# Performance work log

Hardware: AMD Instinct MI355X
Metric: run time of the kernel (lower is better)

Reference implementation:

```python
import jax, jax.numpy as jnp
import numpy as np

CHUNK = 128
TAU = 0.7


def setup_inputs() -> dict:
    key = jax.random.key(0)
    ks = jax.random.split(key, 8)
    B, S, D, H, E = 4, 4096, 2048, 1024, 8
    x = jax.random.normal(ks[0], (B, S, D), dtype=jnp.float32)
    prev_expert_indices = jax.random.randint(ks[1], (B,), 0, E)
    # router MLP params (stored as [in, out]); xavier-uniform-like init, zero biases
    def xavier(k, fin, fout):
        lim = np.sqrt(6.0 / (fin + fout)).astype(np.float32)
        return jax.random.uniform(k, (fin, fout), jnp.float32, -lim, lim)
    w1 = xavier(ks[2], D, H)
    b1 = jnp.zeros((H,), jnp.float32)
    w2 = xavier(ks[3], H, H // 2)
    b2 = jnp.zeros((H // 2,), jnp.float32)
    w3 = jax.random.normal(ks[4], (H // 2, E), jnp.float32) * 0.02  # final layer std=0.02
    b3 = jnp.zeros((E,), jnp.float32)
    return {"x": x, "prev_expert_indices": prev_expert_indices,
            "w1": w1, "b1": b1, "w2": w2, "b2": b2, "w3": w3, "b3": b3}


def reference(x, prev_expert_indices, w1, b1, w2, b2, w3, b3):
    B, S, D = x.shape
    E = w3.shape[1]
    C = S // CHUNK  # num_chunks (seq_len divisible by chunk_size)

    # Router MLP on every token (Dropout is identity in eval), then per-chunk mean
    h = jax.nn.relu(x @ w1 + b1)
    h = jax.nn.relu(h @ w2 + b2)
    tok_logits = h @ w3 + b3                                   # [B, S, E]
    chunk_logits = tok_logits.reshape(B, C, CHUNK, E).mean(2)  # [B, C, E]

    top = jnp.argmax(chunk_logits, axis=-1).astype(jnp.int32)  # [B, C]

    # Sequential hysteresis over chunks (prev_expert_indices given => hysteresis active)
    def step(prev, inp):
        logits_c, top_c, is_first = inp  # [B,E], [B], scalar bool
        cur = jnp.take_along_axis(logits_c, top_c[:, None], axis=1)[:, 0]
        pv = jnp.take_along_axis(logits_c, prev[:, None], axis=1)[:, 0]
        switch = (cur - pv) > TAU
        final = jnp.where(is_first, top_c, jnp.where(switch, top_c, prev))
        flips = jnp.where(is_first, 0, switch.sum().astype(jnp.int32))
        return final, (final, flips)

    is_first = jnp.arange(C) == 0
    _, (experts_t, flips_t) = jax.lax.scan(
        step, jnp.zeros((B,), jnp.int32),
        (chunk_logits.transpose(1, 0, 2), top.T, is_first))
    expert_indices = experts_t.T                               # [B, C]

    one_hot = jax.nn.one_hot(expert_indices, E, dtype=jnp.float32)  # [B, C, E]
    routing_weights = jnp.broadcast_to(one_hot[:, :, None, :],
                                       (B, C, CHUNK, E)).reshape(B, S, E)

    # Stats
    probs = jax.nn.softmax(chunk_logits, axis=-1)
    gate_entropy = -(probs * jnp.log(probs + 1e-8)).sum(-1).mean()
    expert_utilization = one_hot.mean((0, 1))                  # [E]
    flip_rate = flips_t.sum().astype(jnp.float32) / (B * max(1, C - 1))
    routing_concentration = jnp.linalg.norm(expert_utilization)

    return (routing_weights, expert_indices, chunk_logits,
            gate_entropy, expert_utilization, flip_rate, routing_concentration)
```

## Files before the change

kernel.cpp:

```cpp
#include <hip/hip_runtime.h>
#include <math.h>

typedef _Float16 half_t;
typedef __attribute__((ext_vector_type(4))) _Float16 half4v;
typedef __attribute__((ext_vector_type(8))) _Float16 half8v;
typedef __attribute__((ext_vector_type(4))) float floatx4;

constexpr int B_ = 4, S_ = 4096, D_ = 2048, H_ = 1024, H2_ = 512, E_ = 8;
constexpr int CHUNK_ = 128;
constexpr int C_ = S_ / CHUNK_;
constexpr int M_ = B_ * S_;
constexpr float TAU_ = 0.7f;
constexpr float WSCALE = 64.0f, OSCALE = 1.0f / 64.0f;

constexpr int OUT_RW = 0;
constexpr int OUT_EI = OUT_RW + B_ * S_ * E_;
constexpr int OUT_CL = OUT_EI + B_ * C_;
constexpr int OUT_GE = OUT_CL + B_ * C_ * E_;
constexpr int OUT_UT = OUT_GE + 1;
constexpr int OUT_FR = OUT_UT + E_;
constexpr int OUT_RC = OUT_FR + 1;

__global__ __launch_bounds__(256)
void transpose_f16_kernel(const float* __restrict__ W, half_t* __restrict__ outT,
                          int K, int N)
{
    __shared__ float tile[32][33];
    const int tx = threadIdx.x & 31;
    const int ty = threadIdx.x >> 5;
    const int k0 = blockIdx.y * 32;
    const int n0 = blockIdx.x * 32;
#pragma unroll
    for (int r = 0; r < 4; ++r)
        tile[ty + r * 8][tx] = W[(size_t)(k0 + ty + r * 8) * N + n0 + tx];
    __syncthreads();
#pragma unroll
    for (int r = 0; r < 4; ++r)
        outT[(size_t)(n0 + ty + r * 8) * K + k0 + tx] = (half_t)tile[tx][ty + r * 8];
}

__global__ __launch_bounds__(256)
void transpose_split_kernel(const float* __restrict__ W, half_t* __restrict__ hi,
                            half_t* __restrict__ lo, int K, int N)
{
    __shared__ float tile[32][33];
    const int tx = threadIdx.x & 31;
    const int ty = threadIdx.x >> 5;
    const int k0 = blockIdx.y * 32;
    const int n0 = blockIdx.x * 32;
#pragma unroll
    for (int r = 0; r < 4; ++r)
        tile[ty + r * 8][tx] = W[(size_t)(k0 + ty + r * 8) * N + n0 + tx];
    __syncthreads();
#pragma unroll
    for (int r = 0; r < 4; ++r) {
        const float v = tile[tx][ty + r * 8] * WSCALE;
        const half_t h = (half_t)v;
        const size_t off = (size_t)(n0 + ty + r * 8) * K + k0 + tx;
        hi[off] = h;
        lo[off] = (half_t)(v - (float)h);
    }
}

__global__ __launch_bounds__(256, 3)
void gemm1_kernel(const float* __restrict__ X,
                  const half_t* __restrict__ BTh,
                  const float* __restrict__ bias, half_t* __restrict__ outh)
{
    constexpr int KD = D_, ND = H_, BK = 32;
    __shared__ __align__(16) half_t sA[128 * BK];
    __shared__ __align__(16) half_t sB[128 * BK];

    const int tid = threadIdx.x;
    const int lane = tid & 63;
    const int wave = tid >> 6;
    const int wm = (wave & 1) * 64;
    const int wn = (wave >> 1) * 64;
    const int rowBlk = blockIdx.x * 16 + (blockIdx.y >> 3);
    const int colBlk = blockIdx.y & 7;
    const long blockM = (long)rowBlk * 128;
    const long blockN = (long)colBlk * 128;

    floatx4 acc[4][4];
#pragma unroll
    for (int i = 0; i < 4; ++i)
#pragma unroll
        for (int j = 0; j < 4; ++j) acc[i][j] = (floatx4){0.f, 0.f, 0.f, 0.f};

    const int srow = tid >> 2;
    const int skoff = (tid & 3) * 8;
    const int ldsoff = srow * BK + skoff;
    const int fr = lane & 15;
    const int fq = (lane >> 4) * 8;

    const float* Xrow0 = X + (size_t)(blockM + srow) * KD + skoff;
    const float* Xrow1 = Xrow0 + (size_t)64 * KD;

    for (int k0 = 0; k0 < KD; k0 += BK) {
        const float4 a00 = *(const float4*)(Xrow0 + k0);
        const float4 a01 = *(const float4*)(Xrow0 + k0 + 4);
        const float4 a10 = *(const float4*)(Xrow1 + k0);
        const float4 a11 = *(const float4*)(Xrow1 + k0 + 4);
        __syncthreads();
#pragma unroll
        for (int p = 0; p < 2; ++p) {
            const size_t boff = (size_t)(blockN + srow + p * 64) * KD + k0 + skoff;
            __builtin_amdgcn_global_load_lds(
                (const __attribute__((address_space(1))) void*)(BTh + boff),
                (__attribute__((address_space(3))) void*)(sB + ldsoff + p * 2048), 16, 0, 0);
        }
        half8v h0, h1v;
        h0.s0 = (half_t)a00.x; h0.s1 = (half_t)a00.y; h0.s2 = (half_t)a00.z; h0.s3 = (half_t)a00.w;
        h0.s4 = (half_t)a01.x; h0.s5 = (half_t)a01.y; h0.s6 = (half_t)a01.z; h0.s7 = (half_t)a01.w;
        h1v.s0 = (half_t)a10.x; h1v.s1 = (half_t)a10.y; h1v.s2 = (half_t)a10.z; h1v.s3 = (half_t)a10.w;
        h1v.s4 = (half_t)a11.x; h1v.s5 = (half_t)a11.y; h1v.s6 = (half_t)a11.z; h1v.s7 = (half_t)a11.w;
        *(half8v*)(sA + ldsoff) = h0;
        *(half8v*)(sA + ldsoff + 2048) = h1v;
        __syncthreads();

        half8v fb[4];
#pragma unroll
        for (int t = 0; t < 4; ++t)
            fb[t] = *(const half8v*)(sB + (wn + t * 16 + fr) * BK + fq);
#pragma unroll
        for (int i = 0; i < 4; ++i) {
            const half8v fa = *(const half8v*)(sA + (wm + i * 16 + fr) * BK + fq);
#pragma unroll
            for (int j = 0; j < 4; ++j)
                acc[i][j] = __builtin_amdgcn_mfma_f32_16x16x32_f16(fa, fb[j], acc[i][j], 0, 0, 0);
        }
    }

    const int orow = (lane >> 4) * 4;
    const int ocol = lane & 15;
#pragma unroll
    for (int j = 0; j < 4; ++j) {
        const long gn = blockN + wn + j * 16 + ocol;
        const float bj = bias[gn];
#pragma unroll
        for (int i = 0; i < 4; ++i) {
#pragma unroll
            for (int r = 0; r < 4; ++r) {
                const float v = fmaxf(acc[i][j][r] + bj, 0.0f);
                const size_t off = (size_t)(blockM + wm + i * 16 + orow + r) * ND + gn;
                outh[off] = (half_t)v;
            }
        }
    }
}

__global__ __launch_bounds__(256, 3)
void gemm2_fused_kernel(const half_t* __restrict__ Ah,
                        const half_t* __restrict__ BTh, const half_t* __restrict__ BTl,
                        const float* __restrict__ bias, const float* __restrict__ w3,
                        float* __restrict__ cl_acc)
{
    constexpr int KD = H_, BK = 32;
    __shared__ __align__(16) half_t sAh[128 * BK];
    __shared__ __align__(16) half_t sBh[128 * BK];
    __shared__ __align__(16) half_t sBl[128 * BK];

    const int tid = threadIdx.x;
    const int lane = tid & 63;
    const int wave = tid >> 6;
    const int wm = (wave & 1) * 64;
    const int wn = (wave >> 1) * 64;
    const int d = blockIdx.y * 4 + blockIdx.x;
    const int xcd = d & 7;
    const int l = d >> 3;
    const int rowBlk = xcd * 16 + (l >> 2);
    const int colBlk = l & 3;
    const long blockM = (long)rowBlk * 128;
    const long blockN = (long)colBlk * 128;

    floatx4 acc[4][4];
#pragma unroll
    for (int i = 0; i < 4; ++i)
#pragma unroll
        for (int j = 0; j < 4; ++j) acc[i][j] = (floatx4){0.f, 0.f, 0.f, 0.f};

    const int srow = tid >> 2;
    const int skoff = (tid & 3) * 8;
    const int ldsoff = srow * BK + skoff;
    const int fr = lane & 15;
    const int fq = (lane >> 4) * 8;

    for (int k0 = 0; k0 < KD; k0 += BK) {
        __syncthreads();
#pragma unroll
        for (int p = 0; p < 2; ++p) {
            const int row = srow + p * 64;
            const size_t aoff = (size_t)(blockM + row) * KD + k0 + skoff;
            const size_t boff = (size_t)(blockN + row) * KD + k0 + skoff;
            const int loff = ldsoff + p * 2048;
            __builtin_amdgcn_global_load_lds(
                (const __attribute__((address_space(1))) void*)(Ah + aoff),
                (__attribute__((address_space(3))) void*)(sAh + loff), 16, 0, 0);
            __builtin_amdgcn_global_load_lds(
                (const __attribute__((address_space(1))) void*)(BTh + boff),
                (__attribute__((address_space(3))) void*)(sBh + loff), 16, 0, 0);
            __builtin_amdgcn_global_load_lds(
                (const __attribute__((address_space(1))) void*)(BTl + boff),
                (__attribute__((address_space(3))) void*)(sBl + loff), 16, 0, 0);
        }
        __syncthreads();

        half8v fbh[4], fbl[4];
#pragma unroll
        for (int t = 0; t < 4; ++t) {
            fbh[t] = *(const half8v*)(sBh + (wn + t * 16 + fr) * BK + fq);
            fbl[t] = *(const half8v*)(sBl + (wn + t * 16 + fr) * BK + fq);
        }
#pragma unroll
        for (int i = 0; i < 4; ++i) {
            const half8v fah = *(const half8v*)(sAh + (wm + i * 16 + fr) * BK + fq);
#pragma unroll
            for (int j = 0; j < 4; ++j) {
                acc[i][j] = __builtin_amdgcn_mfma_f32_16x16x32_f16(fah, fbh[j], acc[i][j], 0, 0, 0);
                acc[i][j] = __builtin_amdgcn_mfma_f32_16x16x32_f16(fah, fbl[j], acc[i][j], 0, 0, 0);
            }
        }
    }

    const int ocol = lane & 15;
    float p[E_];
#pragma unroll
    for (int e = 0; e < E_; ++e) p[e] = 0.0f;
#pragma unroll
    for (int j = 0; j < 4; ++j) {
        const int gn = (int)blockN + wn + j * 16 + ocol;
        const float bj = bias[gn];
        const float4 w3a = *(const float4*)(w3 + (size_t)gn * E_);
        const float4 w3b = *(const float4*)(w3 + (size_t)gn * E_ + 4);
        float colsum = 0.0f;
#pragma unroll
        for (int i = 0; i < 4; ++i)
#pragma unroll
            for (int r = 0; r < 4; ++r)
                colsum += fmaxf(acc[i][j][r] * OSCALE + bj, 0.0f);
        p[0] += colsum * w3a.x; p[1] += colsum * w3a.y;
        p[2] += colsum * w3a.z; p[3] += colsum * w3a.w;
        p[4] += colsum * w3b.x; p[5] += colsum * w3b.y;
        p[6] += colsum * w3b.z; p[7] += colsum * w3b.w;
    }
#pragma unroll
    for (int e = 0; e < E_; ++e)
#pragma unroll
        for (int off = 32; off > 0; off >>= 1)
            p[e] += __shfl_xor(p[e], off);
#pragma unroll
    for (int e = 0; e < E_; ++e)
        if (lane == e) atomicAdd(&cl_acc[rowBlk * E_ + e], p[e]);
}

__global__ __launch_bounds__(128)
void finalize_kernel(const float* __restrict__ cl_acc, const float* __restrict__ b3,
                     float* __restrict__ out, int* __restrict__ experts_ws)
{
    __shared__ float cl[B_ * C_][E_];
    __shared__ int tops[B_ * C_];
    __shared__ int finals[B_ * C_];
    __shared__ int flips[B_];
    __shared__ float ent[B_ * C_];

    const int tid = threadIdx.x;

    {
        int best = 0;
        float bvv = -1e30f;
#pragma unroll
        for (int e = 0; e < E_; ++e) {
            const float v = cl_acc[tid * E_ + e] * (1.0f / CHUNK_) + b3[e];
            cl[tid][e] = v;
            out[OUT_CL + tid * E_ + e] = v;
            if (v > bvv) { bvv = v; best = e; }
        }
        tops[tid] = best;
    }
    __syncthreads();

    if (tid < B_) {
        const int b = tid;
        int prev = 0, fl = 0;
        for (int c = 0; c < C_; ++c) {
            const int t = tops[b * C_ + c];
            int fin;
            if (c == 0) {
                fin = t;
            } else {
                const float cur = cl[b * C_ + c][t];
                const float pv = cl[b * C_ + c][prev];
                const bool sw = (cur - pv) > TAU_;
                if (sw) fl++;
                fin = sw ? t : prev;
            }
            finals[b * C_ + c] = fin;
            prev = fin;
        }
        flips[b] = fl;
    }

    {
        float m = cl[tid][0];
        for (int e = 1; e < E_; ++e) m = fmaxf(m, cl[tid][e]);
        float pr[E_], s = 0.0f;
        for (int e = 0; e < E_; ++e) { pr[e] = expf(cl[tid][e] - m); s += pr[e]; }
        const float inv = 1.0f / s;
        float h = 0.0f;
        for (int e = 0; e < E_; ++e) { const float pe = pr[e] * inv; h -= pe * logf(pe + 1e-8f); }
        ent[tid] = h;
    }
    __syncthreads();

    if (tid == 0) {
        float esum = 0.0f;
        for (int i = 0; i < B_ * C_; ++i) esum += ent[i];
        out[OUT_GE] = esum / (float)(B_ * C_);

        int cnt[E_];
        for (int e = 0; e < E_; ++e) cnt[e] = 0;
        for (int i = 0; i < B_ * C_; ++i) cnt[finals[i]]++;
        float n2 = 0.0f;
        for (int e = 0; e < E_; ++e) {
            const float u = (float)cnt[e] / (float)(B_ * C_);
            out[OUT_UT + e] = u;
            n2 += u * u;
        }
        const int totfl = flips[0] + flips[1] + flips[2] + flips[3];
        out[OUT_FR] = (float)totfl / (float)(B_ * (C_ - 1));
        out[OUT_RC] = sqrtf(n2);
    }

    out[OUT_EI + tid] = (float)finals[tid];
    experts_ws[tid] = finals[tid];
}

__global__ __launch_bounds__(256)
void routing_weights_kernel(const int* __restrict__ experts_ws, float* __restrict__ out)
{
    const int tok = blockIdx.x * 256 + threadIdx.x;
    const int b = tok >> 12;
    const int c = (tok & (S_ - 1)) >> 7;
    const int e = experts_ws[b * C_ + c];
    float4 v0 = make_float4(e == 0 ? 1.f : 0.f, e == 1 ? 1.f : 0.f,
                            e == 2 ? 1.f : 0.f, e == 3 ? 1.f : 0.f);
    float4 v1 = make_float4(e == 4 ? 1.f : 0.f, e == 5 ? 1.f : 0.f,
                            e == 6 ? 1.f : 0.f, e == 7 ? 1.f : 0.f);
    float4* dst = (float4*)(out + (size_t)tok * E_);
    dst[0] = v0;
    dst[1] = v1;
}

extern "C" void kernel_launch(void* const* d_in, const int* in_sizes, int n_in,
                              void* d_out, int out_size, void* d_ws, size_t ws_size,
                              hipStream_t stream)
{
    const float* x  = (const float*)d_in[0];
    const float* w1 = (const float*)d_in[2];
    const float* b1 = (const float*)d_in[3];
    const float* w2 = (const float*)d_in[4];
    const float* b2 = (const float*)d_in[5];
    const float* w3 = (const float*)d_in[6];
    const float* b3 = (const float*)d_in[7];
    float* out = (float*)d_out;

    half_t* w1t  = (half_t*)d_ws;
    half_t* h1h  = w1t + (size_t)H_ * D_;
    half_t* w2th = h1h + (size_t)M_ * H_;
    half_t* w2tl = w2th + (size_t)H2_ * H_;
    float*  cl_acc = (float*)(w2tl + (size_t)H2_ * H_);
    int* experts_ws = (int*)(cl_acc + B_ * C_ * E_);

    hipMemsetAsync(cl_acc, 0, (size_t)B_ * C_ * E_ * sizeof(float), stream);

    transpose_f16_kernel<<<dim3(H_ / 32, D_ / 32), dim3(256), 0, stream>>>(w1, w1t, D_, H_);
    transpose_split_kernel<<<dim3(H2_ / 32, H_ / 32), dim3(256), 0, stream>>>(w2, w2th, w2tl, H_, H2_);
    gemm1_kernel<<<dim3(H_ / 128, M_ / 128), dim3(256), 0, stream>>>(x, w1t, b1, h1h);
    gemm2_fused_kernel<<<dim3(H2_ / 128, M_ / 128), dim3(256), 0, stream>>>(
        h1h, w2th, w2tl, b2, w3, cl_acc);
    finalize_kernel<<<dim3(1), dim3(128), 0, stream>>>(cl_acc, b3, out, experts_ws);
    routing_weights_kernel<<<dim3(M_ / 256), dim3(256), 0, stream>>>(experts_ws, out + OUT_RW);
}
```

Baseline: 367.2 us.

## Merge prep/finalize kernels and prefetch next X tile in GEMM1

Fuses the two weight-transpose kernels and the accumulator memset into one prep kernel, and merges the finalize and routing-weight kernels into one kernel where every block recomputes the hysteresis scan redundantly. It also software-prefetches the next K-slice of X into registers in gemm1 so global loads overlap the MFMA work. The aim is fewer launches and less exposed load latency, at the cost of redundant per-block scan work and extra register pressure in gemm1.

Result: no change. 364.9 us (-0.6%).

```diff
diff --git a/kernel.cpp b/kernel.cpp
--- a/kernel.cpp
+++ b/kernel.cpp
@@ -2,7 +2,6 @@
 #include <math.h>
 
 typedef _Float16 half_t;
-typedef __attribute__((ext_vector_type(4))) _Float16 half4v;
 typedef __attribute__((ext_vector_type(8))) _Float16 half8v;
 typedef __attribute__((ext_vector_type(4))) float floatx4;
 
@@ -22,43 +21,43 @@
 constexpr int OUT_RC = OUT_FR + 1;
 
 __global__ __launch_bounds__(256)
-void transpose_f16_kernel(const float* __restrict__ W, half_t* __restrict__ outT,
-                          int K, int N)
+void prep_kernel(const float* __restrict__ w1, const float* __restrict__ w2,
+                 half_t* __restrict__ w1t, half_t* __restrict__ w2th,
+                 half_t* __restrict__ w2tl, float* __restrict__ cl_acc)
 {
     __shared__ float tile[32][33];
     const int tx = threadIdx.x & 31;
     const int ty = threadIdx.x >> 5;
-    const int k0 = blockIdx.y * 32;
-    const int n0 = blockIdx.x * 32;
-#pragma unroll
-    for (int r = 0; r < 4; ++r)
-        tile[ty + r * 8][tx] = W[(size_t)(k0 + ty + r * 8) * N + n0 + tx];
-    __syncthreads();
-#pragma unroll
-    for (int r = 0; r < 4; ++r)
-        outT[(size_t)(n0 + ty + r * 8) * K + k0 + tx] = (half_t)tile[tx][ty + r * 8];
-}
-
-__global__ __launch_bounds__(256)
-void transpose_split_kernel(const float* __restrict__ W, half_t* __restrict__ hi,
-                            half_t* __restrict__ lo, int K, int N)
-{
-    __shared__ float tile[32][33];
-    const int tx = threadIdx.x & 31;
-    const int ty = threadIdx.x >> 5;
-    const int k0 = blockIdx.y * 32;
-    const int n0 = blockIdx.x * 32;
-#pragma unroll
-    for (int r = 0; r < 4; ++r)
-        tile[ty + r * 8][tx] = W[(size_t)(k0 + ty + r * 8) * N + n0 + tx];
-    __syncthreads();
-#pragma unroll
-    for (int r = 0; r < 4; ++r) {
-        const float v = tile[tx][ty + r * 8] * WSCALE;
-        const half_t h = (half_t)v;
-        const size_t off = (size_t)(n0 + ty + r * 8) * K + k0 + tx;
-        hi[off] = h;
-        lo[off] = (half_t)(v - (float)h);
+    const int bid = blockIdx.x;
+
+    if (bid < 2048) {
+        const int n0 = (bid & 31) * 32;
+        const int k0 = (bid >> 5) * 32;
+#pragma unroll
+        for (int r = 0; r < 4; ++r)
+            tile[ty + r * 8][tx] = w1[(size_t)(k0 + ty + r * 8) * H_ + n0 + tx];
+        __syncthreads();
+#pragma unroll
+        for (int r = 0; r < 4; ++r)
+            w1t[(size_t)(n0 + ty + r * 8) * D_ + k0 + tx] = (half_t)tile[tx][ty + r * 8];
+    } else if (bid < 2560) {
+        const int b2 = bid - 2048;
+        const int n0 = (b2 & 15) * 32;
+        const int k0 = (b2 >> 4) * 32;
+#pragma unroll
+        for (int r = 0; r < 4; ++r)
+            tile[ty + r * 8][tx] = w2[(size_t)(k0 + ty + r * 8) * H2_ + n0 + tx];
+        __syncthreads();
+#pragma unroll
+        for (int r = 0; r < 4; ++r) {
+            const float v = tile[tx][ty + r * 8] * WSCALE;
+            const half_t h = (half_t)v;
+            const size_t off = (size_t)(n0 + ty + r * 8) * H_ + k0 + tx;
+            w2th[off] = h;
+            w2tl[off] = (half_t)(v - (float)h);
+        }
+    } else {
+        for (int i = threadIdx.x; i < B_ * C_ * E_; i += 256) cl_acc[i] = 0.0f;
     }
 }
 
@@ -96,11 +95,12 @@
     const float* Xrow0 = X + (size_t)(blockM + srow) * KD + skoff;
     const float* Xrow1 = Xrow0 + (size_t)64 * KD;
 
+    float4 a00 = *(const float4*)(Xrow0);
+    float4 a01 = *(const float4*)(Xrow0 + 4);
+    float4 a10 = *(const float4*)(Xrow1);
+    float4 a11 = *(const float4*)(Xrow1 + 4);
+
     for (int k0 = 0; k0 < KD; k0 += BK) {
-        const float4 a00 = *(const float4*)(Xrow0 + k0);
-        const float4 a01 = *(const float4*)(Xrow0 + k0 + 4);
-        const float4 a10 = *(const float4*)(Xrow1 + k0);
-        const float4 a11 = *(const float4*)(Xrow1 + k0 + 4);
         __syncthreads();
 #pragma unroll
         for (int p = 0; p < 2; ++p) {
@@ -116,6 +116,11 @@
         h1v.s4 = (half_t)a11.x; h1v.s5 = (half_t)a11.y; h1v.s6 = (half_t)a11.z; h1v.s7 = (half_t)a11.w;
         *(half8v*)(sA + ldsoff) = h0;
         *(half8v*)(sA + ldsoff + 2048) = h1v;
+        const int kn = (k0 + BK < KD) ? (k0 + BK) : 0;
+        a00 = *(const float4*)(Xrow0 + kn);
+        a01 = *(const float4*)(Xrow0 + kn + 4);
+        a10 = *(const float4*)(Xrow1 + kn);
+        a11 = *(const float4*)(Xrow1 + kn + 4);
         __syncthreads();
 
         half8v fb[4];
@@ -253,9 +258,9 @@
         if (lane == e) atomicAdd(&cl_acc[rowBlk * E_ + e], p[e]);
 }
 
-__global__ __launch_bounds__(128)
-void finalize_kernel(const float* __restrict__ cl_acc, const float* __restrict__ b3,
-                     float* __restrict__ out, int* __restrict__ experts_ws)
+__global__ __launch_bounds__(256)
+void final_route_kernel(const float* __restrict__ cl_acc, const float* __restrict__ b3,
+                        float* __restrict__ out)
 {
     __shared__ float cl[B_ * C_][E_];
     __shared__ int tops[B_ * C_];
@@ -265,14 +270,13 @@
 
     const int tid = threadIdx.x;
 
-    {
+    if (tid < B_ * C_) {
         int best = 0;
         float bvv = -1e30f;
 #pragma unroll
         for (int e = 0; e < E_; ++e) {
             const float v = cl_acc[tid * E_ + e] * (1.0f / CHUNK_) + b3[e];
             cl[tid][e] = v;
-            out[OUT_CL + tid * E_ + e] = v;
             if (v > bvv) { bvv = v; best = e; }
         }
         tops[tid] = best;
@@ -299,56 +303,56 @@
         }
         flips[b] = fl;
     }
+    __syncthreads();
 
     {
-        float m = cl[tid][0];
-        for (int e = 1; e < E_; ++e) m = fmaxf(m, cl[tid][e]);
-        float pr[E_], s = 0.0f;
-        for (int e = 0; e < E_; ++e) { pr[e] = expf(cl[tid][e] - m); s += pr[e]; }
-        const float inv = 1.0f / s;
-        float h = 0.0f;
-        for (int e = 0; e < E_; ++e) { const float pe = pr[e] * inv; h -= pe * logf(pe + 1e-8f); }
-        ent[tid] = h;
-    }
-    __syncthreads();
-
-    if (tid == 0) {
-        float esum = 0.0f;
-        for (int i = 0; i < B_ * C_; ++i) esum += ent[i];
-        out[OUT_GE] = esum / (float)(B_ * C_);
-
-        int cnt[E_];
-        for (int e = 0; e < E_; ++e) cnt[e] = 0;
-        for (int i = 0; i < B_ * C_; ++i) cnt[finals[i]]++;
-        float n2 = 0.0f;
-        for (int e = 0; e < E_; ++e) {
-            const float u = (float)cnt[e] / (float)(B_ * C_);
-            out[OUT_UT + e] = u;
-            n2 += u * u;
-        }
-        const int totfl = flips[0] + flips[1] + flips[2] + flips[3];
-        out[OUT_FR] = (float)totfl / (float)(B_ * (C_ - 1));
-        out[OUT_RC] = sqrtf(n2);
-    }
-
-    out[OUT_EI + tid] = (float)finals[tid];
-    experts_ws[tid] = finals[tid];
-}
-
-__global__ __launch_bounds__(256)
-void routing_weights_kernel(const int* __restrict__ experts_ws, float* __restrict__ out)
-{
-    const int tok = blockIdx.x * 256 + threadIdx.x;
-    const int b = tok >> 12;
-    const int c = (tok & (S_ - 1)) >> 7;
-    const int e = experts_ws[b * C_ + c];
-    float4 v0 = make_float4(e == 0 ? 1.f : 0.f, e == 1 ? 1.f : 0.f,
-                            e == 2 ? 1.f : 0.f, e == 3 ? 1.f : 0.f);
-    float4 v1 = make_float4(e == 4 ? 1.f : 0.f, e == 5 ? 1.f : 0.f,
-                            e == 6 ? 1.f : 0.f, e == 7 ? 1.f : 0.f);
-    float4* dst = (float4*)(out + (size_t)tok * E_);
-    dst[0] = v0;
-    dst[1] = v1;
+        const int tok = blockIdx.x * 256 + tid;
+        const int b = tok >> 12;
+        const int c = (tok & (S_ - 1)) >> 7;
+        const int e = finals[b * C_ + c];
+        float4 v0 = make_float4(e == 0 ? 1.f : 0.f, e == 1 ? 1.f : 0.f,
+                                e == 2 ? 1.f : 0.f, e == 3 ? 1.f : 0.f);
+        float4 v1 = make_float4(e == 4 ? 1.f : 0.f, e == 5 ? 1.f : 0.f,
+                                e == 6 ? 1.f : 0.f, e == 7 ? 1.f : 0.f);
+        float4* dst = (float4*)(out + OUT_RW + (size_t)tok * E_);
+        dst[0] = v0;
+        dst[1] = v1;
+    }
+
+    if (blockIdx.x == 0) {
+        if (tid < B_ * C_) {
+            out[OUT_EI + tid] = (float)finals[tid];
+#pragma unroll
+            for (int e = 0; e < E_; ++e) out[OUT_CL + tid * E_ + e] = cl[tid][e];
+            float m = cl[tid][0];
+            for (int e = 1; e < E_; ++e) m = fmaxf(m, cl[tid][e]);
+            float pr[E_], s = 0.0f;
+            for (int e = 0; e < E_; ++e) { pr[e] = expf(cl[tid][e] - m); s += pr[e]; }
+            const float inv = 1.0f / s;
+            float h = 0.0f;
+            for (int e = 0; e < E_; ++e) { const float pe = pr[e] * inv; h -= pe * logf(pe + 1e-8f); }
+            ent[tid] = h;
+        }
+        __syncthreads();
+        if (tid == 0) {
+            float esum = 0.0f;
+            for (int i = 0; i < B_ * C_; ++i) esum += ent[i];
+            out[OUT_GE] = esum / (float)(B_ * C_);
+
+            int cnt[E_];
+            for (int e = 0; e < E_; ++e) cnt[e] = 0;
+            for (int i = 0; i < B_ * C_; ++i) cnt[finals[i]]++;
+            float n2 = 0.0f;
+            for (int e = 0; e < E_; ++e) {
+                const float u = (float)cnt[e] / (float)(B_ * C_);
+                out[OUT_UT + e] = u;
+                n2 += u * u;
+            }
+            const int totfl = flips[0] + flips[1] + flips[2] + flips[3];
+            out[OUT_FR] = (float)totfl / (float)(B_ * (C_ - 1));
+            out[OUT_RC] = sqrtf(n2);
+        }
+    }
 }
 
 extern "C" void kernel_launch(void* const* d_in, const int* in_sizes, int n_in,
@@ -369,15 +373,10 @@
     half_t* w2th = h1h + (size_t)M_ * H_;
     half_t* w2tl = w2th + (size_t)H2_ * H_;
     float*  cl_acc = (float*)(w2tl + (size_t)H2_ * H_);
-    int* experts_ws = (int*)(cl_acc + B_ * C_ * E_);
-
-    hipMemsetAsync(cl_acc, 0, (size_t)B_ * C_ * E_ * sizeof(float), stream);
-
-    transpose_f16_kernel<<<dim3(H_ / 32, D_ / 32), dim3(256), 0, stream>>>(w1, w1t, D_, H_);
-    transpose_split_kernel<<<dim3(H2_ / 32, H_ / 32), dim3(256), 0, stream>>>(w2, w2th, w2tl, H_, H2_);
+
+    prep_kernel<<<dim3(2561), dim3(256), 0, stream>>>(w1, w2, w1t, w2th, w2tl, cl_acc);
     gemm1_kernel<<<dim3(H_ / 128, M_ / 128), dim3(256), 0, stream>>>(x, w1t, b1, h1h);
     gemm2_fused_kernel<<<dim3(H2_ / 128, M_ / 128), dim3(256), 0, stream>>>(
         h1h, w2th, w2tl, b2, w3, cl_acc);
-    finalize_kernel<<<dim3(1), dim3(128), 0, stream>>>(cl_acc, b3, out, experts_ws);
-    routing_weights_kernel<<<dim3(M_ / 256), dim3(256), 0, stream>>>(experts_ws, out + OUT_RW);
-}
+    final_route_kernel<<<dim3(M_ / 256), dim3(256), 0, stream>>>(cl_acc, b3, out);
+}
```
